# Optimization experiments

Measured on AMD Instinct MI355X. Metric: run time of the kernel, lower is better.

## Reference

```python
import jax, jax.numpy as jnp
import numpy as np

B, DIN, DOUT, Q, H1, H2 = 4096, 768, 512, 64, 32, 64
EPS = 1e-5

def setup_inputs() -> dict:
    key = jax.random.key(0)
    ks = jax.random.split(key, 12)
    s = lambda fan_in: 1.0 / np.sqrt(fan_in)
    return {
        "x": jax.random.normal(ks[0], (B, DIN), jnp.float32),
        # proj_in: Linear(dim_in, dim_out)
        "wp": jax.random.uniform(ks[1], (DIN, DOUT), jnp.float32, -s(DIN), s(DIN)),
        "bp": jax.random.uniform(ks[2], (DOUT,), jnp.float32, -s(DIN), s(DIN)),
        # inner: Linear(1, H1) -> ReLU -> Linear(H1, Q)
        "wi1": jax.random.uniform(ks[3], (H1,), jnp.float32, -1.0, 1.0),
        "bi1": jax.random.uniform(ks[4], (H1,), jnp.float32, -1.0, 1.0),
        "wi2": jax.random.uniform(ks[5], (H1, Q), jnp.float32, -s(H1), s(H1)),
        "bi2": jax.random.uniform(ks[6], (Q,), jnp.float32, -s(H1), s(H1)),
        # outer: Linear(1, H2) -> ReLU -> Linear(H2, dim_out)
        "wo1": jax.random.uniform(ks[7], (H2,), jnp.float32, -1.0, 1.0),
        "bo1": jax.random.uniform(ks[8], (H2,), jnp.float32, -1.0, 1.0),
        "wo2": jax.random.uniform(ks[9], (H2, DOUT), jnp.float32, -s(H2), s(H2)),
        "bo2": jax.random.uniform(ks[10], (DOUT,), jnp.float32, -s(H2), s(H2)),
        # LayerNorm(dim_out)
        "gamma": jnp.ones((DOUT,), jnp.float32),
        "beta": jnp.zeros((DOUT,), jnp.float32),
    }

def _per_scalar_mlp(v, w1, b1, w2, b2):
    # v: [...] scalars -> tiny MLP 1->h->out applied per scalar -> [..., out]
    h = jax.nn.relu(v[..., None] * w1 + b1)          # [..., h]
    return jnp.einsum("...h,ho->...o", h, w2) + b2   # [..., out]

def reference(x, wp, bp, wi1, bi1, wi2, bi2, wo1, bo1, wo2, bo2, gamma, beta):
    x_proj = x @ wp + bp                                    # [B, DOUT]
    inner_out = _per_scalar_mlp(x_proj, wi1, bi1, wi2, bi2)  # [B, DOUT, Q]
    u = inner_out.sum(axis=1)                               # [B, Q]
    outer_out = _per_scalar_mlp(u, wo1, bo1, wo2, bo2)      # [B, Q, DOUT]
    summed = outer_out.sum(axis=1)                          # [B, DOUT]
    mu = summed.mean(axis=-1, keepdims=True)
    var = jnp.var(summed, axis=-1, keepdims=True)
    return (summed - mu) * jax.lax.rsqrt(var + EPS) * gamma + beta
```

## Files before the change

### kernel.cpp

```cpp
#include <hip/hip_runtime.h>
#include <hip/hip_bf16.h>

#define B_ROWS 4096
#define DIN    768
#define DOUT   512
#define QDIM   64
#define H1C    32
#define H2C    64

#define W_BP    0
#define W_WI1   512
#define W_BI1   544
#define W_WI2   576
#define W_BI2   2624
#define W_WO1   2688
#define W_BO1   2752
#define W_WO2   2816
#define W_BO2   35584
#define W_GAM   36096
#define W_BET   36608
#define W_TOT   37120

#define WS_WPT  0
#define WS_WO2T 786432
#define WS_WW   851968

typedef short  short8_t  __attribute__((ext_vector_type(8)));
typedef __bf16 bf16x8_t  __attribute__((ext_vector_type(8)));
typedef float  f32x4_t   __attribute__((ext_vector_type(4)));

__device__ __forceinline__ float bf16bits_to_f32(unsigned short u) {
  return __builtin_bit_cast(float, ((unsigned int)u) << 16);
}
__device__ __forceinline__ unsigned short f32_to_bf16bits(float f) {
  return __builtin_bit_cast(unsigned short, __float2bfloat16(f));
}
__device__ __forceinline__ float ldf(const void* p, int i, bool isb) {
  if (isb) return bf16bits_to_f32(((const unsigned short*)p)[i]);
  return ((const float*)p)[i];
}
__device__ __forceinline__ bool detect_bf16(const unsigned int* xw, int t) {
  const unsigned int w = xw[t & 63];
  const unsigned int e = (w >> 7) & 0xffu;
  const bool hit = (e >= 118u && e <= 127u);
  return __popcll(__ballot(hit)) >= 40;
}

__global__ __launch_bounds__(256) void k_prep(
    const void* __restrict__ x, const void* __restrict__ wp,
    const void* __restrict__ bp,
    const void* __restrict__ wi1, const void* __restrict__ bi1,
    const void* __restrict__ wi2, const void* __restrict__ bi2,
    const void* __restrict__ wo1, const void* __restrict__ bo1,
    const void* __restrict__ wo2, const void* __restrict__ bo2,
    const void* __restrict__ gamma, const void* __restrict__ beta,
    unsigned short* __restrict__ wpT,
    unsigned short* __restrict__ wo2T,
    float* __restrict__ wW)
{
  const int t = threadIdx.x, b = blockIdx.x;
  const bool isb = detect_bf16((const unsigned int*)x, t);
  const int tx = t & 31, ty = t >> 5;

  if (b < 384) {
    __shared__ unsigned short tile[32][33];
    const int n0 = (b & 15) * 32, k0 = (b >> 4) * 32;
#pragma unroll
    for (int i = 0; i < 32; i += 8)
      tile[ty + i][tx] = f32_to_bf16bits(ldf(wp, (k0 + ty + i) * DOUT + n0 + tx, isb));
    __syncthreads();
#pragma unroll
    for (int i = 0; i < 32; i += 8)
      wpT[(size_t)(n0 + ty + i) * DIN + k0 + tx] = tile[tx][ty + i];
  } else if (b < 416) {
    __shared__ unsigned short tile[32][33];
    const int tb = b - 384;
    const int c0 = (tb & 15) * 32, g0 = (tb >> 4) * 32;
#pragma unroll
    for (int i = 0; i < 32; i += 8)
      tile[ty + i][tx] = f32_to_bf16bits(ldf(wo2, (g0 + ty + i) * DOUT + c0 + tx, isb));
    __syncthreads();
#pragma unroll
    for (int i = 0; i < 32; i += 8)
      wo2T[(size_t)(c0 + ty + i) * QDIM + g0 + tx] = tile[tx][ty + i];
  } else {
    for (int e = (b - 416) * 256 + t; e < W_TOT; e += 8 * 256) {
      float v;
      if      (e < W_WI1) v = ldf(bp,    e - W_BP,  isb);
      else if (e < W_BI1) v = ldf(wi1,   e - W_WI1, isb);
      else if (e < W_WI2) v = ldf(bi1,   e - W_BI1, isb);
      else if (e < W_BI2) v = ldf(wi2,   e - W_WI2, isb);
      else if (e < W_WO1) v = ldf(bi2,   e - W_BI2, isb);
      else if (e < W_BO1) v = ldf(wo1,   e - W_WO1, isb);
      else if (e < W_WO2) v = ldf(bo1,   e - W_BO1, isb);
      else if (e < W_BO2) v = ldf(wo2,   e - W_WO2, isb);
      else if (e < W_GAM) v = ldf(bo2,   e - W_BO2, isb);
      else if (e < W_BET) v = ldf(gamma, e - W_GAM, isb);
      else                v = ldf(beta,  e - W_BET, isb);
      wW[e] = v;
    }
  }
}

__global__ __launch_bounds__(1024) void k_main(
    const void* __restrict__ x,
    const unsigned short* __restrict__ wpT,
    const unsigned short* __restrict__ wo2T,
    const float* __restrict__ wW,
    void* __restrict__ out)
{
  __shared__ alignas(16) char smem[43904];
  unsigned short* As   = (unsigned short*)smem;
  float*          sXp  = (float*)smem;
  float*          sS   = (float*)(smem + 33024);
  float*          sU   = (float*)(smem + 35072);
  unsigned short* sTb  = (unsigned short*)(smem + 39168);
  float*          sRed = (float*)(smem + 41472);
  float*          sSt  = (float*)(smem + 43520);
  float*          sW1  = (float*)(smem + 43648);
  float*          sB1  = (float*)(smem + 43776);

  const int t    = threadIdx.x;
  const int wv   = t >> 6, lane = t & 63;
  const int lm   = lane & 15, quad = lane >> 4;
  const int b0   = blockIdx.x * 16;
  const bool isb = detect_bf16((const unsigned int*)x, t);

#pragma unroll
  for (int i = 0; i < 3; ++i) {
    const int c = i * 1024 + t;
    const int row = c / 192, off = (c - row * 192) * 4;
    unsigned short a4[4];
    if (isb) {
      const uint2 v = *(const uint2*)((const unsigned short*)x + (size_t)(b0 + row) * DIN + off);
      *(uint2*)a4 = v;
    } else {
      const float4 f = *(const float4*)((const float*)x + (size_t)(b0 + row) * DIN + off);
      a4[0] = f32_to_bf16bits(f.x); a4[1] = f32_to_bf16bits(f.y);
      a4[2] = f32_to_bf16bits(f.z); a4[3] = f32_to_bf16bits(f.w);
    }
    *(uint2*)&As[row * 776 + off] = *(const uint2*)a4;
  }
  if (t < 32) { sW1[t] = wW[W_WI1 + t]; sB1[t] = wW[W_BI1 + t]; }

  const unsigned short* wb0 = wpT + (size_t)(wv * 32 + lm) * DIN + quad * 8;
  const unsigned short* wb1 = wb0 + 16 * DIN;
  short8_t c0 = *(const short8_t*)wb0;
  short8_t c1 = *(const short8_t*)wb1;
  short8_t n0 = *(const short8_t*)(wb0 + 32);
  short8_t n1 = *(const short8_t*)(wb1 + 32);
  __syncthreads();

  f32x4_t acc0 = {}, acc1 = {};
#pragma unroll
  for (int kt = 0; kt < 24; ++kt) {
    const short8_t f0 = *(const short8_t*)(wb0 + (kt + 2) * 32);
    const short8_t f1 = *(const short8_t*)(wb1 + (kt + 2) * 32);
    const short8_t av = *(const short8_t*)&As[lm * 776 + kt * 32 + quad * 8];
    const bf16x8_t af = __builtin_bit_cast(bf16x8_t, av);
    acc0 = __builtin_amdgcn_mfma_f32_16x16x32_bf16(af, __builtin_bit_cast(bf16x8_t, c0), acc0, 0, 0, 0);
    acc1 = __builtin_amdgcn_mfma_f32_16x16x32_bf16(af, __builtin_bit_cast(bf16x8_t, c1), acc1, 0, 0, 0);
    c0 = n0; c1 = n1; n0 = f0; n1 = f1;
  }
  __syncthreads();

  {
    const int ca = wv * 32 + lm, cb = ca + 16;
    const float bpa = wW[W_BP + ca], bpb = wW[W_BP + cb];
#pragma unroll
    for (int i = 0; i < 4; ++i) {
      sXp[(quad * 4 + i) * 516 + ca] = acc0[i] + bpa;
      sXp[(quad * 4 + i) * 516 + cb] = acc1[i] + bpb;
    }
  }
  __syncthreads();

  {
    const int r = wv, cg = lane & 31, hg = lane >> 5;
    const float* row = &sXp[r * 516 + cg * 16];
    float xc[16];
#pragma unroll
    for (int j = 0; j < 4; ++j) {
      const float4 v = *(const float4*)&row[j * 4];
      xc[j*4+0] = v.x; xc[j*4+1] = v.y; xc[j*4+2] = v.z; xc[j*4+3] = v.w;
    }
    float S16[16];
#pragma unroll
    for (int j = 0; j < 16; ++j) {
      const float w = sW1[hg * 16 + j], bb = sB1[hg * 16 + j];
      float a = 0.f;
#pragma unroll
      for (int c = 0; c < 16; ++c) a += fmaxf(fmaf(xc[c], w, bb), 0.f);
      S16[j] = a;
    }
#pragma unroll
    for (int off = 1; off < 32; off <<= 1)
#pragma unroll
      for (int j = 0; j < 16; ++j) S16[j] += __shfl_xor(S16[j], off);
    if (cg == 0) {
#pragma unroll
      for (int j = 0; j < 16; ++j) sS[r * 32 + hg * 16 + j] = S16[j];
    }
  }
  __syncthreads();

  {
    const int r = t >> 6, q = t & 63;
    float a = 0.f;
#pragma unroll
    for (int h4 = 0; h4 < 32; h4 += 4) {
      const float4 s4 = *(const float4*)&sS[r * 32 + h4];
      a = fmaf(s4.x, wW[W_WI2 + (h4 + 0) * QDIM + q], a);
      a = fmaf(s4.y, wW[W_WI2 + (h4 + 1) * QDIM + q], a);
      a = fmaf(s4.z, wW[W_WI2 + (h4 + 2) * QDIM + q], a);
      a = fmaf(s4.w, wW[W_WI2 + (h4 + 3) * QDIM + q], a);
    }
    sU[t] = a + 512.f * wW[W_BI2 + q];
  }
  __syncthreads();

  {
    const int r = t >> 6, g = t & 63;
    const float w = wW[W_WO1 + g], bb = wW[W_BO1 + g];
    float a = 0.f;
#pragma unroll
    for (int q = 0; q < QDIM; q += 4) {
      const float4 v = *(const float4*)&sU[r * 64 + q];
      a += fmaxf(fmaf(v.x, w, bb), 0.f);
      a += fmaxf(fmaf(v.y, w, bb), 0.f);
      a += fmaxf(fmaf(v.z, w, bb), 0.f);
      a += fmaxf(fmaf(v.w, w, bb), 0.f);
    }
    sTb[r * 72 + g] = f32_to_bf16bits(a);
  }
  __syncthreads();

  f32x4_t sa0 = {}, sa1 = {};
  {
    const unsigned short* wcol0 = wo2T + (size_t)(wv * 32 + lm) * QDIM + quad * 8;
    const unsigned short* wcol1 = wcol0 + 16 * QDIM;
#pragma unroll
    for (int kt = 0; kt < 2; ++kt) {
      const short8_t aT = *(const short8_t*)&sTb[lm * 72 + kt * 32 + quad * 8];
      const bf16x8_t aTf = __builtin_bit_cast(bf16x8_t, aT);
      const short8_t bW0 = *(const short8_t*)(wcol0 + kt * 32);
      const short8_t bW1 = *(const short8_t*)(wcol1 + kt * 32);
      sa0 = __builtin_amdgcn_mfma_f32_16x16x32_bf16(aTf, __builtin_bit_cast(bf16x8_t, bW0), sa0, 0, 0, 0);
      sa1 = __builtin_amdgcn_mfma_f32_16x16x32_bf16(aTf, __builtin_bit_cast(bf16x8_t, bW1), sa1, 0, 0, 0);
    }
  }
  const int colA = wv * 32 + lm, colB = colA + 16;
  {
    const float bzA = 64.f * wW[W_BO2 + colA];
    const float bzB = 64.f * wW[W_BO2 + colB];
#pragma unroll
    for (int i = 0; i < 4; ++i) { sa0[i] += bzA; sa1[i] += bzB; }
  }
  {
    float pr[4], prs[4];
#pragma unroll
    for (int i = 0; i < 4; ++i) {
      pr[i]  = sa0[i] + sa1[i];
      prs[i] = sa0[i] * sa0[i] + sa1[i] * sa1[i];
    }
#pragma unroll
    for (int off = 1; off < 16; off <<= 1)
#pragma unroll
      for (int i = 0; i < 4; ++i) {
        pr[i]  += __shfl_xor(pr[i],  off);
        prs[i] += __shfl_xor(prs[i], off);
      }
    if (lm == 0) {
#pragma unroll
      for (int i = 0; i < 4; ++i) {
        sRed[(wv * 16 + quad * 4 + i) * 2 + 0] = pr[i];
        sRed[(wv * 16 + quad * 4 + i) * 2 + 1] = prs[i];
      }
    }
  }
  __syncthreads();
  if (t < 16) {
    float sm = 0.f, sq = 0.f;
#pragma unroll
    for (int w = 0; w < 16; ++w) {
      sm += sRed[(w * 16 + t) * 2 + 0];
      sq += sRed[(w * 16 + t) * 2 + 1];
    }
    const float mu  = sm * (1.f / 512.f);
    const float var = fmaxf(sq * (1.f / 512.f) - mu * mu, 0.f);
    sSt[t * 2 + 0] = mu;
    sSt[t * 2 + 1] = rsqrtf(var + 1e-5f);
  }
  __syncthreads();

  {
    const float gA = wW[W_GAM + colA], bA = wW[W_BET + colA];
    const float gB = wW[W_GAM + colB], bB = wW[W_BET + colB];
#pragma unroll
    for (int i = 0; i < 4; ++i) {
      const int r = quad * 4 + i;
      const float mu = sSt[r * 2 + 0], rstd = sSt[r * 2 + 1];
      const float oA = (sa0[i] - mu) * rstd * gA + bA;
      const float oB = (sa1[i] - mu) * rstd * gB + bB;
      if (isb) {
        ((unsigned short*)out)[(size_t)(b0 + r) * DOUT + colA] = f32_to_bf16bits(oA);
        ((unsigned short*)out)[(size_t)(b0 + r) * DOUT + colB] = f32_to_bf16bits(oB);
      } else {
        ((float*)out)[(size_t)(b0 + r) * DOUT + colA] = oA;
        ((float*)out)[(size_t)(b0 + r) * DOUT + colB] = oB;
      }
    }
  }
}

extern "C" void kernel_launch(void* const* d_in, const int* in_sizes, int n_in,
                              void* d_out, int out_size, void* d_ws, size_t ws_size,
                              hipStream_t stream) {
  char* ws = (char*)d_ws;
  unsigned short* wpT  = (unsigned short*)(ws + WS_WPT);
  unsigned short* wo2T = (unsigned short*)(ws + WS_WO2T);
  float*          wW   = (float*)(ws + WS_WW);

  k_prep<<<424, 256, 0, stream>>>(d_in[0], d_in[1], d_in[2], d_in[3], d_in[4],
                                  d_in[5], d_in[6], d_in[7], d_in[8], d_in[9],
                                  d_in[10], d_in[11], d_in[12], wpT, wo2T, wW);
  k_main<<<B_ROWS / 16, 1024, 0, stream>>>(d_in[0], wpT, wo2T, wW, d_out);
}
```

Baseline: 136.6 us.

## Halve block to 512 threads with four N-tiles per wave in main kernel

The main kernel now runs 8 waves of 512 threads instead of 16, and each wave computes 64 output columns (four 16-wide MFMA tiles) rather than 32. Each A fragment loaded from LDS therefore feeds four MFMAs, and the elementwise stages loop twice per thread. Launch bounds allow two blocks per CU to make up for the fewer waves per block. In exchange, register pressure rises from the extra accumulators and prefetch buffers, and per-block latency may grow.

```diff
diff --git a/kernel.cpp b/kernel.cpp
--- a/kernel.cpp
+++ b/kernel.cpp
@@ -102,23 +102,23 @@
   }
 }
 
-__global__ __launch_bounds__(1024) void k_main(
+__global__ __launch_bounds__(512, 2) void k_main(
     const void* __restrict__ x,
     const unsigned short* __restrict__ wpT,
     const unsigned short* __restrict__ wo2T,
     const float* __restrict__ wW,
     void* __restrict__ out)
 {
-  __shared__ alignas(16) char smem[43904];
+  __shared__ alignas(16) char smem[42880];
   unsigned short* As   = (unsigned short*)smem;
   float*          sXp  = (float*)smem;
   float*          sS   = (float*)(smem + 33024);
   float*          sU   = (float*)(smem + 35072);
   unsigned short* sTb  = (unsigned short*)(smem + 39168);
   float*          sRed = (float*)(smem + 41472);
-  float*          sSt  = (float*)(smem + 43520);
-  float*          sW1  = (float*)(smem + 43648);
-  float*          sB1  = (float*)(smem + 43776);
+  float*          sSt  = (float*)(smem + 42496);
+  float*          sW1  = (float*)(smem + 42624);
+  float*          sB1  = (float*)(smem + 42752);
 
   const int t    = threadIdx.x;
   const int wv   = t >> 6, lane = t & 63;
@@ -127,13 +127,12 @@
   const bool isb = detect_bf16((const unsigned int*)x, t);
 
 #pragma unroll
-  for (int i = 0; i < 3; ++i) {
-    const int c = i * 1024 + t;
+  for (int i = 0; i < 6; ++i) {
+    const int c = i * 512 + t;
     const int row = c / 192, off = (c - row * 192) * 4;
     unsigned short a4[4];
     if (isb) {
-      const uint2 v = *(const uint2*)((const unsigned short*)x + (size_t)(b0 + row) * DIN + off);
-      *(uint2*)a4 = v;
+      *(uint2*)a4 = *(const uint2*)((const unsigned short*)x + (size_t)(b0 + row) * DIN + off);
     } else {
       const float4 f = *(const float4*)((const float*)x + (size_t)(b0 + row) * DIN + off);
       a4[0] = f32_to_bf16bits(f.x); a4[1] = f32_to_bf16bits(f.y);
@@ -143,69 +142,81 @@
   }
   if (t < 32) { sW1[t] = wW[W_WI1 + t]; sB1[t] = wW[W_BI1 + t]; }
 
-  const unsigned short* wb0 = wpT + (size_t)(wv * 32 + lm) * DIN + quad * 8;
-  const unsigned short* wb1 = wb0 + 16 * DIN;
-  short8_t c0 = *(const short8_t*)wb0;
-  short8_t c1 = *(const short8_t*)wb1;
-  short8_t n0 = *(const short8_t*)(wb0 + 32);
-  short8_t n1 = *(const short8_t*)(wb1 + 32);
-  __syncthreads();
-
-  f32x4_t acc0 = {}, acc1 = {};
+  const unsigned short* wb[4];
+  short8_t cur[4], nxt[4];
+#pragma unroll
+  for (int nt = 0; nt < 4; ++nt) {
+    wb[nt] = wpT + (size_t)(wv * 64 + nt * 16 + lm) * DIN + quad * 8;
+    cur[nt] = *(const short8_t*)wb[nt];
+    nxt[nt] = *(const short8_t*)(wb[nt] + 32);
+  }
+  __syncthreads();
+
+  f32x4_t acc[4] = {};
 #pragma unroll
   for (int kt = 0; kt < 24; ++kt) {
-    const short8_t f0 = *(const short8_t*)(wb0 + (kt + 2) * 32);
-    const short8_t f1 = *(const short8_t*)(wb1 + (kt + 2) * 32);
+    short8_t fut[4];
+#pragma unroll
+    for (int nt = 0; nt < 4; ++nt)
+      fut[nt] = *(const short8_t*)(wb[nt] + (kt + 2) * 32);
     const short8_t av = *(const short8_t*)&As[lm * 776 + kt * 32 + quad * 8];
     const bf16x8_t af = __builtin_bit_cast(bf16x8_t, av);
-    acc0 = __builtin_amdgcn_mfma_f32_16x16x32_bf16(af, __builtin_bit_cast(bf16x8_t, c0), acc0, 0, 0, 0);
-    acc1 = __builtin_amdgcn_mfma_f32_16x16x32_bf16(af, __builtin_bit_cast(bf16x8_t, c1), acc1, 0, 0, 0);
-    c0 = n0; c1 = n1; n0 = f0; n1 = f1;
+#pragma unroll
+    for (int nt = 0; nt < 4; ++nt)
+      acc[nt] = __builtin_amdgcn_mfma_f32_16x16x32_bf16(
+          af, __builtin_bit_cast(bf16x8_t, cur[nt]), acc[nt], 0, 0, 0);
+#pragma unroll
+    for (int nt = 0; nt < 4; ++nt) { cur[nt] = nxt[nt]; nxt[nt] = fut[nt]; }
+  }
+  __syncthreads();
+
+#pragma unroll
+  for (int nt = 0; nt < 4; ++nt) {
+    const int col = wv * 64 + nt * 16 + lm;
+    const float bpv = wW[W_BP + col];
+#pragma unroll
+    for (int i = 0; i < 4; ++i)
+      sXp[(quad * 4 + i) * 516 + col] = acc[nt][i] + bpv;
   }
   __syncthreads();
 
   {
-    const int ca = wv * 32 + lm, cb = ca + 16;
-    const float bpa = wW[W_BP + ca], bpb = wW[W_BP + cb];
-#pragma unroll
-    for (int i = 0; i < 4; ++i) {
-      sXp[(quad * 4 + i) * 516 + ca] = acc0[i] + bpa;
-      sXp[(quad * 4 + i) * 516 + cb] = acc1[i] + bpb;
-    }
-  }
-  __syncthreads();
-
-  {
-    const int r = wv, cg = lane & 31, hg = lane >> 5;
-    const float* row = &sXp[r * 516 + cg * 16];
-    float xc[16];
-#pragma unroll
-    for (int j = 0; j < 4; ++j) {
-      const float4 v = *(const float4*)&row[j * 4];
-      xc[j*4+0] = v.x; xc[j*4+1] = v.y; xc[j*4+2] = v.z; xc[j*4+3] = v.w;
-    }
-    float S16[16];
-#pragma unroll
-    for (int j = 0; j < 16; ++j) {
-      const float w = sW1[hg * 16 + j], bb = sB1[hg * 16 + j];
-      float a = 0.f;
-#pragma unroll
-      for (int c = 0; c < 16; ++c) a += fmaxf(fmaf(xc[c], w, bb), 0.f);
-      S16[j] = a;
-    }
-#pragma unroll
-    for (int off = 1; off < 32; off <<= 1)
-#pragma unroll
-      for (int j = 0; j < 16; ++j) S16[j] += __shfl_xor(S16[j], off);
-    if (cg == 0) {
-#pragma unroll
-      for (int j = 0; j < 16; ++j) sS[r * 32 + hg * 16 + j] = S16[j];
-    }
-  }
-  __syncthreads();
-
-  {
-    const int r = t >> 6, q = t & 63;
+    const int cg = lane & 31, hg = lane >> 5;
+#pragma unroll
+    for (int half = 0; half < 2; ++half) {
+      const int r = wv * 2 + half;
+      const float* row = &sXp[r * 516 + cg * 16];
+      float xc[16];
+#pragma unroll
+      for (int j = 0; j < 4; ++j) {
+        const float4 v = *(const float4*)&row[j * 4];
+        xc[j*4+0] = v.x; xc[j*4+1] = v.y; xc[j*4+2] = v.z; xc[j*4+3] = v.w;
+      }
+      float S16[16];
+#pragma unroll
+      for (int j = 0; j < 16; ++j) {
+        const float w = sW1[hg * 16 + j], bb = sB1[hg * 16 + j];
+        float a = 0.f;
+#pragma unroll
+        for (int c = 0; c < 16; ++c) a += fmaxf(fmaf(xc[c], w, bb), 0.f);
+        S16[j] = a;
+      }
+#pragma unroll
+      for (int off = 1; off < 32; off <<= 1)
+#pragma unroll
+        for (int j = 0; j < 16; ++j) S16[j] += __shfl_xor(S16[j], off);
+      if (cg == 0) {
+#pragma unroll
+        for (int j = 0; j < 16; ++j) sS[r * 32 + hg * 16 + j] = S16[j];
+      }
+    }
+  }
+  __syncthreads();
+
+#pragma unroll
+  for (int rep = 0; rep < 2; ++rep) {
+    const int e = rep * 512 + t;
+    const int r = e >> 6, q = e & 63;
     float a = 0.f;
 #pragma unroll
     for (int h4 = 0; h4 < 32; h4 += 4) {
@@ -215,12 +226,14 @@
       a = fmaf(s4.z, wW[W_WI2 + (h4 + 2) * QDIM + q], a);
       a = fmaf(s4.w, wW[W_WI2 + (h4 + 3) * QDIM + q], a);
     }
-    sU[t] = a + 512.f * wW[W_BI2 + q];
-  }
-  __syncthreads();
-
-  {
-    const int r = t >> 6, g = t & 63;
+    sU[e] = a + 512.f * wW[W_BI2 + q];
+  }
+  __syncthreads();
+
+#pragma unroll
+  for (int rep = 0; rep < 2; ++rep) {
+    const int e = rep * 512 + t;
+    const int r = e >> 6, g = e & 63;
     const float w = wW[W_WO1 + g], bb = wW[W_BO1 + g];
     float a = 0.f;
 #pragma unroll
@@ -235,33 +248,34 @@
   }
   __syncthreads();
 
-  f32x4_t sa0 = {}, sa1 = {};
-  {
-    const unsigned short* wcol0 = wo2T + (size_t)(wv * 32 + lm) * QDIM + quad * 8;
-    const unsigned short* wcol1 = wcol0 + 16 * QDIM;
-#pragma unroll
-    for (int kt = 0; kt < 2; ++kt) {
-      const short8_t aT = *(const short8_t*)&sTb[lm * 72 + kt * 32 + quad * 8];
-      const bf16x8_t aTf = __builtin_bit_cast(bf16x8_t, aT);
-      const short8_t bW0 = *(const short8_t*)(wcol0 + kt * 32);
-      const short8_t bW1 = *(const short8_t*)(wcol1 + kt * 32);
-      sa0 = __builtin_amdgcn_mfma_f32_16x16x32_bf16(aTf, __builtin_bit_cast(bf16x8_t, bW0), sa0, 0, 0, 0);
-      sa1 = __builtin_amdgcn_mfma_f32_16x16x32_bf16(aTf, __builtin_bit_cast(bf16x8_t, bW1), sa1, 0, 0, 0);
-    }
-  }
-  const int colA = wv * 32 + lm, colB = colA + 16;
-  {
-    const float bzA = 64.f * wW[W_BO2 + colA];
-    const float bzB = 64.f * wW[W_BO2 + colB];
-#pragma unroll
-    for (int i = 0; i < 4; ++i) { sa0[i] += bzA; sa1[i] += bzB; }
-  }
+  f32x4_t sa[4] = {};
+#pragma unroll
+  for (int kt = 0; kt < 2; ++kt) {
+    const short8_t aT = *(const short8_t*)&sTb[lm * 72 + kt * 32 + quad * 8];
+    const bf16x8_t aTf = __builtin_bit_cast(bf16x8_t, aT);
+#pragma unroll
+    for (int nt = 0; nt < 4; ++nt) {
+      const short8_t bW = *(const short8_t*)
+          (wo2T + (size_t)(wv * 64 + nt * 16 + lm) * QDIM + kt * 32 + quad * 8);
+      sa[nt] = __builtin_amdgcn_mfma_f32_16x16x32_bf16(
+          aTf, __builtin_bit_cast(bf16x8_t, bW), sa[nt], 0, 0, 0);
+    }
+  }
+#pragma unroll
+  for (int nt = 0; nt < 4; ++nt) {
+    const float bz = 64.f * wW[W_BO2 + wv * 64 + nt * 16 + lm];
+#pragma unroll
+    for (int i = 0; i < 4; ++i) sa[nt][i] += bz;
+  }
+
   {
     float pr[4], prs[4];
 #pragma unroll
     for (int i = 0; i < 4; ++i) {
-      pr[i]  = sa0[i] + sa1[i];
-      prs[i] = sa0[i] * sa0[i] + sa1[i] * sa1[i];
+      float s = 0.f, s2 = 0.f;
+#pragma unroll
+      for (int nt = 0; nt < 4; ++nt) { s += sa[nt][i]; s2 += sa[nt][i] * sa[nt][i]; }
+      pr[i] = s; prs[i] = s2;
     }
 #pragma unroll
     for (int off = 1; off < 16; off <<= 1)
@@ -282,7 +296,7 @@
   if (t < 16) {
     float sm = 0.f, sq = 0.f;
 #pragma unroll
-    for (int w = 0; w < 16; ++w) {
+    for (int w = 0; w < 8; ++w) {
       sm += sRed[(w * 16 + t) * 2 + 0];
       sq += sRed[(w * 16 + t) * 2 + 1];
     }
@@ -293,22 +307,18 @@
   }
   __syncthreads();
 
-  {
-    const float gA = wW[W_GAM + colA], bA = wW[W_BET + colA];
-    const float gB = wW[W_GAM + colB], bB = wW[W_BET + colB];
+#pragma unroll
+  for (int nt = 0; nt < 4; ++nt) {
+    const int col = wv * 64 + nt * 16 + lm;
+    const float gm = wW[W_GAM + col], bt = wW[W_BET + col];
 #pragma unroll
     for (int i = 0; i < 4; ++i) {
       const int r = quad * 4 + i;
-      const float mu = sSt[r * 2 + 0], rstd = sSt[r * 2 + 1];
-      const float oA = (sa0[i] - mu) * rstd * gA + bA;
-      const float oB = (sa1[i] - mu) * rstd * gB + bB;
-      if (isb) {
-        ((unsigned short*)out)[(size_t)(b0 + r) * DOUT + colA] = f32_to_bf16bits(oA);
-        ((unsigned short*)out)[(size_t)(b0 + r) * DOUT + colB] = f32_to_bf16bits(oB);
-      } else {
-        ((float*)out)[(size_t)(b0 + r) * DOUT + colA] = oA;
-        ((float*)out)[(size_t)(b0 + r) * DOUT + colB] = oB;
-      }
+      const float o = (sa[nt][i] - sSt[r * 2 + 0]) * sSt[r * 2 + 1] * gm + bt;
+      if (isb)
+        ((unsigned short*)out)[(size_t)(b0 + r) * DOUT + col] = f32_to_bf16bits(o);
+      else
+        ((float*)out)[(size_t)(b0 + r) * DOUT + col] = o;
     }
   }
 }
@@ -324,5 +334,5 @@
   k_prep<<<424, 256, 0, stream>>>(d_in[0], d_in[1], d_in[2], d_in[3], d_in[4],
                                   d_in[5], d_in[6], d_in[7], d_in[8], d_in[9],
                                   d_in[10], d_in[11], d_in[12], wpT, wo2T, wW);
-  k_main<<<B_ROWS / 16, 1024, 0, stream>>>(d_in[0], wpT, wo2T, wW, d_out);
-}
+  k_main<<<B_ROWS / 16, 512, 0, stream>>>(d_in[0], wpT, wo2T, wW, d_out);
+}
```

After: 129.8 us. -5.0%, faster.
